# Optimization experiments

Hardware: AMD Instinct MI355X
Metric: run time of the kernel (lower is better)

The kernel has to match this reference:

```python
import jax, jax.numpy as jnp
import numpy as np

HEADS = 4
DIM_HEAD = 32
SCALE = DIM_HEAD ** -0.5


def setup_inputs() -> dict:
    key = jax.random.key(0)
    k1, k2, k3 = jax.random.split(key, 3)
    dim = 128
    hidden = HEADS * DIM_HEAD  # 128
    x = jax.random.normal(k1, (4, dim, 64, 64), dtype=jnp.float32)
    w_qkv = jax.random.normal(k2, (3 * hidden, dim), dtype=jnp.float32) * (dim ** -0.5)
    w_out = jax.random.normal(k3, (dim, hidden), dtype=jnp.float32) * (hidden ** -0.5)
    b_out = jnp.zeros((dim,), dtype=jnp.float32)
    return {"x": x, "w_qkv": w_qkv, "w_out": w_out, "b_out": b_out}


def reference(x, w_qkv, w_out, b_out):
    b, c, h, w = x.shape
    n = h * w
    # 1x1 conv == channel matmul per pixel
    qkv = jnp.einsum('oc,bchw->bohw', w_qkv, x)  # [b, 3*hidden, h, w]
    q, k, v = jnp.split(qkv, 3, axis=1)
    # b (heads d) x y -> b heads d (x y)
    def to_heads(t):
        return t.reshape(b, HEADS, DIM_HEAD, n)
    q = to_heads(q) * SCALE
    k = to_heads(k)
    v = to_heads(v)
    sim = jnp.einsum('bhdi,bhdj->bhij', q, k)          # [b, heads, n, n]
    attn = jax.nn.softmax(sim, axis=-1)
    out = jnp.einsum('bhij,bhdj->bhid', attn, v)        # [b, heads, n, d]
    # b h (x y) d -> b (h d) x y
    out = out.transpose(0, 1, 3, 2).reshape(b, HEADS * DIM_HEAD, h, w)
    out = jnp.einsum('oc,bchw->bohw', w_out, out) + b_out[None, :, None, None]
    return out
```

## Files before the change

kernel.cpp:

```cpp
#include <hip/hip_runtime.h>
#include <math.h>

#define NHEAD 4
#define DHEAD 32
#define NPIX  4096
#define CIN   128

typedef __bf16 bf16_t;
typedef __bf16 bf16x8 __attribute__((ext_vector_type(8)));
typedef __bf16 bf16x4 __attribute__((ext_vector_type(4)));
typedef float  f32x4  __attribute__((ext_vector_type(4)));

constexpr float QSCALE = 0.17677669529663687f * 1.4426950408889634f;

__global__ void __launch_bounds__(384) qkv_mfma(
    const float* __restrict__ x, const float* __restrict__ wqkv,
    ushort* __restrict__ qb, ushort* __restrict__ kb, ushort* __restrict__ vT) {
  __shared__ ushort Xls[32 * 136];
  const int tid = threadIdx.x, cg = tid >> 6, lane = tid & 63;
  const int n = lane & 15, quad = lane >> 4;
  const int b = blockIdx.y, p0 = blockIdx.x * 32;

  const float wsc = (cg < 2) ? QSCALE : 1.0f;
  bf16x8 wf[4][4];
#pragma unroll
  for (int t1 = 0; t1 < 4; ++t1)
#pragma unroll
    for (int k = 0; k < 4; ++k) {
      const float* wp = wqkv + (size_t)(cg * 64 + t1 * 16 + n) * CIN + k * 32 + quad * 8;
      float4 a = *(const float4*)wp;
      float4 c = *(const float4*)(wp + 4);
      wf[t1][k] = (bf16x8){(bf16_t)(a.x * wsc), (bf16_t)(a.y * wsc),
                           (bf16_t)(a.z * wsc), (bf16_t)(a.w * wsc),
                           (bf16_t)(c.x * wsc), (bf16_t)(c.y * wsc),
                           (bf16_t)(c.z * wsc), (bf16_t)(c.w * wsc)};
    }

  if (tid < 256) {
    const int pc = tid & 7;
    const int c  = (tid >> 3) * 4;
    const float* xp = x + ((size_t)b * CIN + c) * NPIX + p0 + pc * 4;
    float4 r0 = *(const float4*)xp;
    float4 r1 = *(const float4*)(xp + NPIX);
    float4 r2 = *(const float4*)(xp + 2 * NPIX);
    float4 r3 = *(const float4*)(xp + 3 * NPIX);
    bf16x4 w0 = {(bf16_t)r0.x, (bf16_t)r1.x, (bf16_t)r2.x, (bf16_t)r3.x};
    bf16x4 w1 = {(bf16_t)r0.y, (bf16_t)r1.y, (bf16_t)r2.y, (bf16_t)r3.y};
    bf16x4 w2 = {(bf16_t)r0.z, (bf16_t)r1.z, (bf16_t)r2.z, (bf16_t)r3.z};
    bf16x4 w3 = {(bf16_t)r0.w, (bf16_t)r1.w, (bf16_t)r2.w, (bf16_t)r3.w};
    *(bf16x4*)&Xls[(pc * 4 + 0) * 136 + c] = w0;
    *(bf16x4*)&Xls[(pc * 4 + 1) * 136 + c] = w1;
    *(bf16x4*)&Xls[(pc * 4 + 2) * 136 + c] = w2;
    *(bf16x4*)&Xls[(pc * 4 + 3) * 136 + c] = w3;
  }
  __syncthreads();

  f32x4 acc[4][2];
#pragma unroll
  for (int i = 0; i < 4; ++i)
#pragma unroll
    for (int j = 0; j < 2; ++j) acc[i][j] = (f32x4){0.f, 0.f, 0.f, 0.f};

  const bool isv = (cg >= 4);
#pragma unroll
  for (int k = 0; k < 4; ++k) {
    bf16x8 xf[2];
#pragma unroll
    for (int pt = 0; pt < 2; ++pt)
      xf[pt] = *(const bf16x8*)&Xls[(pt * 16 + n) * 136 + k * 32 + quad * 8];
    if (!isv) {
#pragma unroll
      for (int wt = 0; wt < 4; ++wt)
#pragma unroll
        for (int pt = 0; pt < 2; ++pt)
          acc[wt][pt] = __builtin_amdgcn_mfma_f32_16x16x32_bf16(
              wf[wt][k], xf[pt], acc[wt][pt], 0, 0, 0);
    } else {
#pragma unroll
      for (int ct = 0; ct < 4; ++ct)
#pragma unroll
        for (int pt = 0; pt < 2; ++pt)
          acc[ct][pt] = __builtin_amdgcn_mfma_f32_16x16x32_bf16(
              xf[pt], wf[ct][k], acc[ct][pt], 0, 0, 0);
    }
  }

  if (!isv) {
    ushort* dst0 = (cg < 2) ? qb : kb;
#pragma unroll
    for (int wt = 0; wt < 4; ++wt) {
      const int ch = (cg & 1) * 64 + wt * 16 + quad * 4;
      const int head = ch >> 5, d = ch & 31;
#pragma unroll
      for (int pt = 0; pt < 2; ++pt) {
        const int p = p0 + pt * 16 + n;
        f32x4 a = acc[wt][pt];
        bf16x4 o = {(bf16_t)a[0], (bf16_t)a[1], (bf16_t)a[2], (bf16_t)a[3]};
        *(bf16x4*)(dst0 + ((size_t)(b * NHEAD + head) * NPIX + p) * DHEAD + d) = o;
      }
    }
  } else {
#pragma unroll
    for (int ct = 0; ct < 4; ++ct) {
      const int ch = (cg & 1) * 64 + ct * 16 + n;
      const int head = ch >> 5, d = ch & 31;
#pragma unroll
      for (int pt = 0; pt < 2; ++pt) {
        const int p = p0 + pt * 16 + quad * 4;
        f32x4 a = acc[ct][pt];
        bf16x4 o = {(bf16_t)a[0], (bf16_t)a[1], (bf16_t)a[2], (bf16_t)a[3]};
        *(bf16x4*)(vT + ((size_t)(b * NHEAD + head) * DHEAD + d) * NPIX + p) = o;
      }
    }
  }
}

__device__ __forceinline__ void fl_load(const ushort* kb0, const ushort* vb0,
                                        int st, bf16x8* f) {
  f[0] = *(const bf16x8*)(kb0 + (size_t)(st * 32) * DHEAD);
  f[1] = *(const bf16x8*)(kb0 + (size_t)(st * 32 + 4) * DHEAD);
  f[2] = *(const bf16x8*)(vb0 + st * 32);
  f[3] = *(const bf16x8*)(vb0 + (size_t)16 * NPIX + st * 32);
}

__device__ __forceinline__ void fl_compute(const bf16x8* qf, const bf16x8* f,
                                           const bf16x8 ones,
                                           f32x4 O[4][2], f32x4* Ol) {
  const f32x4 zero = {0.f, 0.f, 0.f, 0.f};
#pragma unroll
  for (int rp = 0; rp < 4; ++rp) {
    f32x4 sa = __builtin_amdgcn_mfma_f32_16x16x32_bf16(f[0], qf[rp], zero, 0, 0, 0);
    f32x4 sb = __builtin_amdgcn_mfma_f32_16x16x32_bf16(f[1], qf[rp], zero, 0, 0, 0);
    bf16x8 pf;
#pragma unroll
    for (int r = 0; r < 4; ++r) {
      pf[r]     = (bf16_t)__builtin_amdgcn_exp2f(sa[r]);
      pf[r + 4] = (bf16_t)__builtin_amdgcn_exp2f(sb[r]);
    }
    O[rp][0] = __builtin_amdgcn_mfma_f32_16x16x32_bf16(pf, f[2], O[rp][0], 0, 0, 0);
    O[rp][1] = __builtin_amdgcn_mfma_f32_16x16x32_bf16(pf, f[3], O[rp][1], 0, 0, 0);
    Ol[rp]   = __builtin_amdgcn_mfma_f32_16x16x32_bf16(pf, ones, Ol[rp], 0, 0, 0);
  }
}

__global__ void __launch_bounds__(256, 4) flash_mfma(
    const ushort* __restrict__ qb, const ushort* __restrict__ kbuf,
    const ushort* __restrict__ vTb, ushort* __restrict__ aoT) {
  __shared__ float Ols[4][64][34];
  const int tid = threadIdx.x, wave = tid >> 6, lane = tid & 63;
  const int n = lane & 15, quad = lane >> 4;
  const int id = blockIdx.x;
  const int bh = (id & 7) * 2 + ((id >> 3) & 1);
  const int q0 = (id >> 4) * 64;

  const ushort* kg = kbuf + (size_t)bh * NPIX * DHEAD;
  const ushort* vg = vTb + (size_t)bh * DHEAD * NPIX;

  bf16x8 qf[4];
#pragma unroll
  for (int rp = 0; rp < 4; ++rp)
    qf[rp] = *(const bf16x8*)(qb +
        ((size_t)bh * NPIX + q0 + rp * 16 + n) * DHEAD + quad * 8);

  f32x4 O[4][2], Ol[4];
#pragma unroll
  for (int rp = 0; rp < 4; ++rp) {
    O[rp][0] = (f32x4){0.f, 0.f, 0.f, 0.f};
    O[rp][1] = (f32x4){0.f, 0.f, 0.f, 0.f};
    Ol[rp]   = (f32x4){0.f, 0.f, 0.f, 0.f};
  }
  const bf16_t one = (bf16_t)1.0f;
  const bf16x8 ones = {one, one, one, one, one, one, one, one};

  const int pk = ((n >> 2) << 3) | (n & 3);
  const ushort* kb0 = kg + (size_t)(wave * 1024 + pk) * DHEAD + quad * 8;
  const ushort* vb0 = vg + (size_t)n * NPIX + wave * 1024 + quad * 8;

  bf16x8 fA[4], fB[4];
  fl_load(kb0, vb0, 0, fA);
#pragma unroll 1
  for (int st = 0; st < 32; st += 2) {
    fl_load(kb0, vb0, st + 1, fB);
    fl_compute(qf, fA, ones, O, Ol);
    if (st + 2 < 32) fl_load(kb0, vb0, st + 2, fA);
    fl_compute(qf, fB, ones, O, Ol);
  }

  float* W = &Ols[wave][0][0];
#pragma unroll
  for (int rp = 0; rp < 4; ++rp)
#pragma unroll
    for (int r = 0; r < 4; ++r) {
      const int q = rp * 16 + quad * 4 + r;
      W[q * 34 + n]      = O[rp][0][r];
      W[q * 34 + 16 + n] = O[rp][1][r];
      if (n == 0) W[q * 34 + 32] = Ol[rp][r];
    }
  __syncthreads();

  const int q = tid >> 2, dg = tid & 3;
  const float l = Ols[0][q][32] + Ols[1][q][32] + Ols[2][q][32] + Ols[3][q][32];
  const float inv = 1.f / l;
  bf16x8 o8;
#pragma unroll
  for (int e = 0; e < 8; ++e) {
    const int d = dg * 8 + e;
    const float s = Ols[0][q][d] + Ols[1][q][d] + Ols[2][q][d] + Ols[3][q][d];
    o8[e] = (bf16_t)(s * inv);
  }
  *(bf16x8*)(aoT + ((size_t)bh * NPIX + q0 + q) * DHEAD + dg * 8) = o8;
}

__global__ void __launch_bounds__(256) out_mfma(
    const ushort* __restrict__ aoT, const float* __restrict__ wout,
    const float* __restrict__ bias, float* __restrict__ out) {
  const int tid = threadIdx.x, wv = tid >> 6, lane = tid & 63;
  const int n = lane & 15, quad = lane >> 4;
  const int b = blockIdx.y;
  const int oc0 = (wv & 1) * 64;
  const int p = blockIdx.x * 32 + (wv >> 1) * 16 + n;

  bf16x8 wf[4][4];
#pragma unroll
  for (int mt = 0; mt < 4; ++mt)
#pragma unroll
    for (int k = 0; k < 4; ++k) {
      const float* wp = wout + (size_t)(oc0 + mt * 16 + n) * CIN + k * 32 + quad * 8;
      float4 a = *(const float4*)wp;
      float4 c = *(const float4*)(wp + 4);
      wf[mt][k] = (bf16x8){(bf16_t)a.x, (bf16_t)a.y, (bf16_t)a.z, (bf16_t)a.w,
                           (bf16_t)c.x, (bf16_t)c.y, (bf16_t)c.z, (bf16_t)c.w};
    }

  bf16x8 bfr[4];
#pragma unroll
  for (int k = 0; k < 4; ++k)
    bfr[k] = *(const bf16x8*)(aoT + ((size_t)(b * NHEAD + k) * NPIX + p) * DHEAD + quad * 8);

  f32x4 acc[4];
#pragma unroll
  for (int mt = 0; mt < 4; ++mt) acc[mt] = (f32x4){0.f, 0.f, 0.f, 0.f};
#pragma unroll
  for (int k = 0; k < 4; ++k)
#pragma unroll
    for (int mt = 0; mt < 4; ++mt)
      acc[mt] = __builtin_amdgcn_mfma_f32_16x16x32_bf16(wf[mt][k], bfr[k], acc[mt], 0, 0, 0);

#pragma unroll
  for (int mt = 0; mt < 4; ++mt) {
    const int oc = oc0 + mt * 16 + quad * 4;
#pragma unroll
    for (int r = 0; r < 4; ++r)
      out[((size_t)b * CIN + oc + r) * NPIX + p] = acc[mt][r] + bias[oc + r];
  }
}

extern "C" void kernel_launch(void* const* d_in, const int* in_sizes, int n_in,
                              void* d_out, int out_size, void* d_ws, size_t ws_size,
                              hipStream_t stream) {
  const float* x     = (const float*)d_in[0];
  const float* w_qkv = (const float*)d_in[1];
  const float* w_out = (const float*)d_in[2];
  const float* b_out = (const float*)d_in[3];
  float* out = (float*)d_out;

  char* base = (char*)d_ws;
  ushort* qb  = (ushort*)base;
  ushort* kb  = (ushort*)(base + (size_t)4 * 1024 * 1024);
  ushort* vT  = (ushort*)(base + (size_t)8 * 1024 * 1024);
  ushort* aoT = (ushort*)(base + (size_t)12 * 1024 * 1024);

  qkv_mfma<<<dim3(128, 4), 384, 0, stream>>>(x, w_qkv, qb, kb, vT);
  flash_mfma<<<dim3(1024), 256, 0, stream>>>(qb, kb, vT, aoT);
  out_mfma<<<dim3(128, 4), 256, 0, stream>>>(aoT, w_out, b_out, out);
}
```

Baseline: 140.2 us.

## Halve flash query tile to 32 rows and double grid, restructure MFMA batching

```diff
diff --git a/kernel.cpp b/kernel.cpp
--- a/kernel.cpp
+++ b/kernel.cpp
@@ -125,46 +125,53 @@
 
 __device__ __forceinline__ void fl_compute(const bf16x8* qf, const bf16x8* f,
                                            const bf16x8 ones,
-                                           f32x4 O[4][2], f32x4* Ol) {
+                                           f32x4 O[2][2], f32x4* Ol) {
   const f32x4 zero = {0.f, 0.f, 0.f, 0.f};
-#pragma unroll
-  for (int rp = 0; rp < 4; ++rp) {
-    f32x4 sa = __builtin_amdgcn_mfma_f32_16x16x32_bf16(f[0], qf[rp], zero, 0, 0, 0);
-    f32x4 sb = __builtin_amdgcn_mfma_f32_16x16x32_bf16(f[1], qf[rp], zero, 0, 0, 0);
-    bf16x8 pf;
+  f32x4 s[2][2];
+#pragma unroll
+  for (int rp = 0; rp < 2; ++rp) {
+    s[rp][0] = __builtin_amdgcn_mfma_f32_16x16x32_bf16(f[0], qf[rp], zero, 0, 0, 0);
+    s[rp][1] = __builtin_amdgcn_mfma_f32_16x16x32_bf16(f[1], qf[rp], zero, 0, 0, 0);
+  }
+  bf16x8 pf[2];
+#pragma unroll
+  for (int rp = 0; rp < 2; ++rp) {
 #pragma unroll
     for (int r = 0; r < 4; ++r) {
-      pf[r]     = (bf16_t)__builtin_amdgcn_exp2f(sa[r]);
-      pf[r + 4] = (bf16_t)__builtin_amdgcn_exp2f(sb[r]);
-    }
-    O[rp][0] = __builtin_amdgcn_mfma_f32_16x16x32_bf16(pf, f[2], O[rp][0], 0, 0, 0);
-    O[rp][1] = __builtin_amdgcn_mfma_f32_16x16x32_bf16(pf, f[3], O[rp][1], 0, 0, 0);
-    Ol[rp]   = __builtin_amdgcn_mfma_f32_16x16x32_bf16(pf, ones, Ol[rp], 0, 0, 0);
-  }
-}
-
-__global__ void __launch_bounds__(256, 4) flash_mfma(
+      pf[rp][r]     = (bf16_t)__builtin_amdgcn_exp2f(s[rp][0][r]);
+      pf[rp][r + 4] = (bf16_t)__builtin_amdgcn_exp2f(s[rp][1][r]);
+    }
+  }
+#pragma unroll
+  for (int rp = 0; rp < 2; ++rp) {
+    O[rp][0] = __builtin_amdgcn_mfma_f32_16x16x32_bf16(pf[rp], f[2], O[rp][0], 0, 0, 0);
+    O[rp][1] = __builtin_amdgcn_mfma_f32_16x16x32_bf16(pf[rp], f[3], O[rp][1], 0, 0, 0);
+    Ol[rp]   = __builtin_amdgcn_mfma_f32_16x16x32_bf16(pf[rp], ones, Ol[rp], 0, 0, 0);
+  }
+}
+
+__global__ void __launch_bounds__(256, 5) flash_mfma(
     const ushort* __restrict__ qb, const ushort* __restrict__ kbuf,
     const ushort* __restrict__ vTb, ushort* __restrict__ aoT) {
-  __shared__ float Ols[4][64][34];
+  __shared__ float Ols[4][32][34];
   const int tid = threadIdx.x, wave = tid >> 6, lane = tid & 63;
   const int n = lane & 15, quad = lane >> 4;
   const int id = blockIdx.x;
   const int bh = (id & 7) * 2 + ((id >> 3) & 1);
-  const int q0 = (id >> 4) * 64;
+  const int q0 = (id >> 4) * 32;
 
   const ushort* kg = kbuf + (size_t)bh * NPIX * DHEAD;
   const ushort* vg = vTb + (size_t)bh * DHEAD * NPIX;
 
-  bf16x8 qf[4];
-#pragma unroll
-  for (int rp = 0; rp < 4; ++rp)
+  bf16x8 qf[2];
+#pragma unroll
+  for (int rp = 0; rp < 2; ++rp)
     qf[rp] = *(const bf16x8*)(qb +
         ((size_t)bh * NPIX + q0 + rp * 16 + n) * DHEAD + quad * 8);
 
-  f32x4 O[4][2], Ol[4];
-#pragma unroll
-  for (int rp = 0; rp < 4; ++rp) {
+  f32x4 O[2][2], Ol[2];
+#pragma unroll
+  for (int rp = 0; rp < 2; ++rp) {
     O[rp][0] = (f32x4){0.f, 0.f, 0.f, 0.f};
     O[rp][1] = (f32x4){0.f, 0.f, 0.f, 0.f};
     Ol[rp]   = (f32x4){0.f, 0.f, 0.f, 0.f};
@@ -188,7 +195,7 @@
 
   float* W = &Ols[wave][0][0];
 #pragma unroll
-  for (int rp = 0; rp < 4; ++rp)
+  for (int rp = 0; rp < 2; ++rp)
 #pragma unroll
     for (int r = 0; r < 4; ++r) {
       const int q = rp * 16 + quad * 4 + r;
@@ -198,17 +205,18 @@
     }
   __syncthreads();
 
-  const int q = tid >> 2, dg = tid & 3;
+  const int q = tid >> 3, dg = tid & 7;
   const float l = Ols[0][q][32] + Ols[1][q][32] + Ols[2][q][32] + Ols[3][q][32];
   const float inv = 1.f / l;
-  bf16x8 o8;
-#pragma unroll
-  for (int e = 0; e < 8; ++e) {
-    const int d = dg * 8 + e;
-    const float s = Ols[0][q][d] + Ols[1][q][d] + Ols[2][q][d] + Ols[3][q][d];
-    o8[e] = (bf16_t)(s * inv);
-  }
-  *(bf16x8*)(aoT + ((size_t)bh * NPIX + q0 + q) * DHEAD + dg * 8) = o8;
+  f32x4 s0 = *(f32x4*)&Ols[0][q][dg * 4];
+  f32x4 s1 = *(f32x4*)&Ols[1][q][dg * 4];
+  f32x4 s2 = *(f32x4*)&Ols[2][q][dg * 4];
+  f32x4 s3 = *(f32x4*)&Ols[3][q][dg * 4];
+  bf16x4 o4 = {(bf16_t)((s0[0] + s1[0] + s2[0] + s3[0]) * inv),
+               (bf16_t)((s0[1] + s1[1] + s2[1] + s3[1]) * inv),
+               (bf16_t)((s0[2] + s1[2] + s2[2] + s3[2]) * inv),
+               (bf16_t)((s0[3] + s1[3] + s2[3] + s3[3]) * inv)};
+  *(bf16x4*)(aoT + ((size_t)bh * NPIX + q0 + q) * DHEAD + dg * 4) = o4;
 }
 
 __global__ void __launch_bounds__(256) out_mfma(
@@ -271,6 +279,6 @@
   ushort* aoT = (ushort*)(base + (size_t)12 * 1024 * 1024);
 
   qkv_mfma<<<dim3(128, 4), 384, 0, stream>>>(x, w_qkv, qb, kb, vT);
-  flash_mfma<<<dim3(1024), 256, 0, stream>>>(qb, kb, vT, aoT);
+  flash_mfma<<<dim3(2048), 256, 0, stream>>>(qb, kb, vT, aoT);
   out_mfma<<<dim3(128, 4), 256, 0, stream>>>(aoT, w_out, b_out, out);
 }
```

New measurement: 179.7 us. 28.2% more time.
